# Kernel tuning notes

Hardware: AMD Instinct MI355X
Metric: run time of the kernel (lower is better)

Reference implementation:

```python
import jax, jax.numpy as jnp
import numpy as np

N_NODES = 100000
N_EDGES = 3200000
N_GRAPHS = 1024
D = 64
STEPS_PROP = 6
STEPS_S2S = 6


def setup_inputs() -> dict:
    key = jax.random.key(0)
    ks = jax.random.split(key, 16)
    inp = {}
    inp['x'] = jax.random.normal(ks[0], (N_NODES, 15), dtype=jnp.float32)
    inp['edge_index'] = jax.random.randint(ks[1], (2, N_EDGES), 0, N_NODES, dtype=jnp.int64 if jax.config.jax_enable_x64 else jnp.int32)
    inp['batch'] = jnp.sort(jax.random.randint(ks[2], (N_NODES,), 0, N_GRAPHS, dtype=jnp.int64 if jax.config.jax_enable_x64 else jnp.int32))
    s = 0.1
    inp['W0'] = jax.random.normal(ks[3], (15, D), dtype=jnp.float32) * s
    inp['b0'] = jax.random.normal(ks[4], (D,), dtype=jnp.float32) * s
    inp['Wc'] = jax.random.normal(ks[5], (D, D), dtype=jnp.float32) * s
    inp['bc'] = jax.random.normal(ks[6], (D,), dtype=jnp.float32) * s
    inp['Wih'] = jax.random.normal(ks[7], (4 * D, 2 * D), dtype=jnp.float32) * s
    inp['Whh'] = jax.random.normal(ks[8], (4 * D, D), dtype=jnp.float32) * s
    inp['bih'] = jax.random.normal(ks[9], (4 * D,), dtype=jnp.float32) * s
    inp['bhh'] = jax.random.normal(ks[10], (4 * D,), dtype=jnp.float32) * s
    inp['W1'] = jax.random.normal(ks[11], (2 * D, D), dtype=jnp.float32) * s
    inp['b1'] = jax.random.normal(ks[12], (D,), dtype=jnp.float32) * s
    inp['W2'] = jax.random.normal(ks[13], (D, 12), dtype=jnp.float32) * s
    inp['b2'] = jax.random.normal(ks[14], (12,), dtype=jnp.float32) * s
    return inp


def _gcn_forward(x, edge_index, batch, W0, b0, Wc, bc, Wih, Whh, bih, bhh, W1, b1, W2, b2):
    N = x.shape[0]
    # GCNConv normalization with self-loops (PyG semantics): A_hat = D^-1/2 (A+I) D^-1/2
    loops = jnp.arange(N, dtype=edge_index.dtype)
    row = jnp.concatenate([edge_index[0], loops])  # source
    col = jnp.concatenate([edge_index[1], loops])  # target
    deg = jax.ops.segment_sum(jnp.ones_like(col, dtype=x.dtype), col, num_segments=N)
    dinv = jnp.where(deg > 0, jax.lax.rsqrt(jnp.maximum(deg, 1e-30)), 0.0)
    norm = dinv[row] * dinv[col]  # [E+N]

    out = jax.nn.relu(x @ W0 + b0)  # [N, D]
    for _ in range(STEPS_PROP):
        h = out @ Wc  # transform first
        msg = h[row] * norm[:, None]  # gather along edges
        out = jax.nn.relu(jax.ops.segment_sum(msg, col, num_segments=N) + bc)

    # Set2Set pooling
    B = N_GRAPHS
    d = out.shape[1]
    h_l = jnp.zeros((B, d), dtype=out.dtype)
    c_l = jnp.zeros((B, d), dtype=out.dtype)
    q_star = jnp.zeros((B, 2 * d), dtype=out.dtype)
    for _ in range(STEPS_S2S):
        gates = q_star @ Wih.T + h_l @ Whh.T + bih + bhh  # [B, 4d]
        i_g, f_g, g_g, o_g = jnp.split(gates, 4, axis=1)
        c_l = jax.nn.sigmoid(f_g) * c_l + jax.nn.sigmoid(i_g) * jnp.tanh(g_g)
        h_l = jax.nn.sigmoid(o_g) * jnp.tanh(c_l)
        q = h_l  # [B, d]
        e = jnp.sum(out * q[batch], axis=-1)  # [N]
        m = jax.ops.segment_max(e, batch, num_segments=B)
        a_num = jnp.exp(e - m[batch])
        denom = jax.ops.segment_sum(a_num, batch, num_segments=B)
        a = a_num / denom[batch]
        r = jax.ops.segment_sum(a[:, None] * out, batch, num_segments=B)  # [B, d]
        q_star = jnp.concatenate([q, r], axis=-1)

    y = jax.nn.relu(q_star @ W1 + b1)
    return y @ W2 + b2  # [B, 12]


def reference(x, edge_index, batch, W0, b0, Wc, bc, Wih, Whh, bih, bhh, W1, b1, W2, b2):
    return _gcn_forward(x, edge_index, batch, W0, b0, Wc, bc, Wih, Whh, bih, bhh, W1, b1, W2, b2)
```

## Files before the change

kernel.cpp:

```cpp
#include <hip/hip_runtime.h>
#include <hip/hip_fp16.h>
#include <math.h>

#define ND 64
constexpr int BKT_SHIFT = 9;
constexpr int BKT_MASK = (1 << BKT_SHIFT) - 1;
constexpr int BCUR_PAD = 16;
constexpr int STG_TILE = 8192;
constexpr int S2S_CAP = 144;

__device__ __forceinline__ float sigmoidf_(float x){ return 1.f/(1.f+__expf(-x)); }
__device__ __forceinline__ __half2 h2lo(uint2 v){ return *reinterpret_cast<__half2*>(&v.x); }
__device__ __forceinline__ __half2 h2hi(uint2 v){ return *reinterpret_cast<__half2*>(&v.y); }
__device__ __forceinline__ __half2 shxor_h2(__half2 h, int off){
  unsigned u = *reinterpret_cast<unsigned*>(&h);
  u = __shfl_xor(u, off, 64);
  return *reinterpret_cast<__half2*>(&u);
}

__global__ void k_bhist(const int* __restrict__ col, int* __restrict__ bgcnt,
                        int E, int NBK){
  __shared__ int lhist[512];
  int t0 = blockIdx.x * STG_TILE;
  int t1 = t0 + STG_TILE; if (t1 > E) t1 = E;
  for (int i = threadIdx.x; i < NBK; i += 256) lhist[i] = 0;
  __syncthreads();
  for (int i = t0 + threadIdx.x; i < t1; i += 256)
    atomicAdd(&lhist[col[i] >> BKT_SHIFT], 1);
  __syncthreads();
  for (int i = threadIdx.x; i < NBK; i += 256)
    if (lhist[i] > 0) atomicAdd(&bgcnt[i], lhist[i]);
}

__global__ void k_bscan(const int* __restrict__ bgcnt, int* __restrict__ bstart,
                        int* __restrict__ rowptr, int NBK, int E, int N){
  __shared__ int tmp[256];
  int t = threadIdx.x;
  int v = (t < NBK) ? bgcnt[t] : 0;
  tmp[t] = v; __syncthreads();
  for (int off=1; off<256; off<<=1){
    int u = (t>=off) ? tmp[t-off] : 0;
    __syncthreads();
    tmp[t] += u;
    __syncthreads();
  }
  if (t <= NBK) bstart[t] = (t==0) ? 0 : tmp[t-1];
  if (t == 0) rowptr[N] = E;
}

__global__ void k_bcinit(const int* __restrict__ bstart, int* __restrict__ bcur, int NBK){
  int b = blockIdx.x*blockDim.x + threadIdx.x;
  if (b < NBK) bcur[b*BCUR_PAD] = bstart[b];
}

__global__ void k_stage2(const int* __restrict__ row, const int* __restrict__ col,
                         int* __restrict__ bcur, unsigned* __restrict__ pairs,
                         int E, int NBK){
  __shared__ int lhist[512];
  __shared__ int lbase[512];
  int t0 = blockIdx.x * STG_TILE;
  int t1 = t0 + STG_TILE; if (t1 > E) t1 = E;
  for (int i = threadIdx.x; i < NBK; i += 256) lhist[i] = 0;
  __syncthreads();
  for (int i = t0 + threadIdx.x; i < t1; i += 256)
    atomicAdd(&lhist[col[i] >> BKT_SHIFT], 1);
  __syncthreads();
  for (int i = threadIdx.x; i < NBK; i += 256){
    int c = lhist[i];
    lbase[i] = (c > 0) ? atomicAdd(&bcur[i*BCUR_PAD], c) : 0;
    lhist[i] = 0;
  }
  __syncthreads();
  for (int i = t0 + threadIdx.x; i < t1; i += 256){
    int d = col[i];
    int b = d >> BKT_SHIFT;
    int pos = lbase[b] + atomicAdd(&lhist[b], 1);
    pairs[pos] = ((unsigned)row[i] << BKT_SHIFT) | (unsigned)(d & BKT_MASK);
  }
}

__global__ void k_place(const unsigned* __restrict__ pairs, const int* __restrict__ bstart,
                        int* __restrict__ rowptr, float* __restrict__ dinv,
                        int* __restrict__ csr, int N){
  __shared__ int h[1 << BKT_SHIFT];
  __shared__ int excl[1 << BKT_SHIFT];
  __shared__ int tsum[256];
  int b = blockIdx.x;
  int base = b << BKT_SHIFT;
  int nend = base + (1 << BKT_SHIFT); if (nend > N) nend = N;
  int cnt = nend - base;
  int t = threadIdx.x;
  int s = bstart[b], e = bstart[b+1];

  h[2*t] = 0; h[2*t+1] = 0;
  __syncthreads();
  for (int i = s + t; i < e; i += 256)
    atomicAdd(&h[pairs[i] & BKT_MASK], 1);
  __syncthreads();
  int a0 = h[2*t], a1 = h[2*t+1];
  tsum[t] = a0 + a1;
  __syncthreads();
  for (int off=1; off<256; off<<=1){
    int u = (t>=off) ? tsum[t-off] : 0;
    __syncthreads();
    tsum[t] += u;
    __syncthreads();
  }
  int base0 = (t==0) ? 0 : tsum[t-1];
  excl[2*t]   = base0;
  excl[2*t+1] = base0 + a0;
  __syncthreads();
  for (int c = t; c < cnt; c += 256){
    int deg = h[c];
    rowptr[base + c] = s + excl[c];
    dinv[base + c] = rsqrtf((float)(deg + 1));
  }
  __syncthreads();
  for (int c = t; c < cnt; c += 256) h[c] = s + excl[c];
  __syncthreads();
  for (int i = s + t; i < e; i += 256){
    unsigned p = pairs[i];
    int pos = atomicAdd(&h[p & BKT_MASK], 1);
    csr[pos] = (int)(p >> BKT_SHIFT);
  }
}

__global__ void k_input(const float* __restrict__ x, const float* __restrict__ W0,
                        const float* __restrict__ b0, const float* __restrict__ dinv,
                        __half* __restrict__ s, int N){
  __shared__ float w0s[15*ND];
  __shared__ float b0s[ND];
  int tid = threadIdx.x;
  for (int i=tid; i<15*ND; i+=256) w0s[i] = W0[i];
  if (tid < ND) b0s[tid] = b0[tid];
  __syncthreads();
  int node = blockIdx.x*4 + (tid>>6);
  int f = tid & 63;
  if (node < N){
    float acc = b0s[f];
    const float* xr = x + (size_t)node*15;
    #pragma unroll
    for (int k=0;k<15;k++) acc += xr[k]*w0s[k*ND+f];
    s[(size_t)node*ND+f] = __float2half_rn(dinv[node]*fmaxf(acc, 0.f));
  }
}

__global__ void k_prop(const __half* __restrict__ sbuf, const int* __restrict__ rowptr,
                       const int* __restrict__ csr, const float* __restrict__ dinv,
                       const float* __restrict__ Wc, const float* __restrict__ bc,
                       __half* __restrict__ s_new, __half* __restrict__ outh,
                       int N, int wout){
  __shared__ float wcs[ND*ND];
  __shared__ float xs[16][ND];
  __shared__ float bcs[ND];
  const uint2* g8 = (const uint2*)sbuf;
  int tid = threadIdx.x;
  for (int i=tid; i<ND*ND; i+=256) wcs[i] = Wc[i];
  if (tid < ND) bcs[tid] = bc[tid];
  int nb = blockIdx.x*16;
  int wv = tid>>6, lane = tid&63;
  int grp = lane>>4, li = lane&15;

  for (int q=0; q<4; ++q){
    int node = nb + wv*4 + q;
    float val = 0.f;
    if (node < N){
      int s = rowptr[node], e = rowptr[node+1];
      __half2 z = __float2half2_rn(0.f);
      __half2 a0x=z,a0y=z, a1x=z,a1y=z, a2x=z,a2y=z, a3x=z,a3y=z;
      int i = s;
      for (; i + 16 <= e; i += 16){
        int s0 = csr[i +  0 + grp];
        int s1 = csr[i +  4 + grp];
        int s2 = csr[i +  8 + grp];
        int s3 = csr[i + 12 + grp];
        uint2 v0 = g8[(size_t)s0*16 + li];
        uint2 v1 = g8[(size_t)s1*16 + li];
        uint2 v2 = g8[(size_t)s2*16 + li];
        uint2 v3 = g8[(size_t)s3*16 + li];
        a0x = __hadd2(a0x, h2lo(v0)); a0y = __hadd2(a0y, h2hi(v0));
        a1x = __hadd2(a1x, h2lo(v1)); a1y = __hadd2(a1y, h2hi(v1));
        a2x = __hadd2(a2x, h2lo(v2)); a2y = __hadd2(a2y, h2hi(v2));
        a3x = __hadd2(a3x, h2lo(v3)); a3y = __hadd2(a3y, h2hi(v3));
      }
      for (; i + 4 <= e; i += 4){
        int s0 = csr[i + grp];
        uint2 v0 = g8[(size_t)s0*16 + li];
        a0x = __hadd2(a0x, h2lo(v0)); a0y = __hadd2(a0y, h2hi(v0));
      }
      int r = e - i;
      if (grp < r){
        int s0 = csr[i + grp];
        uint2 v0 = g8[(size_t)s0*16 + li];
        a1x = __hadd2(a1x, h2lo(v0)); a1y = __hadd2(a1y, h2hi(v0));
      }
      __half2 sxh = __hadd2(__hadd2(a0x,a1x), __hadd2(a2x,a3x));
      __half2 syh = __hadd2(__hadd2(a0y,a1y), __hadd2(a2y,a3y));
      sxh = __hadd2(sxh, shxor_h2(sxh, 16));
      syh = __hadd2(syh, shxor_h2(syh, 16));
      sxh = __hadd2(sxh, shxor_h2(sxh, 32));
      syh = __hadd2(syh, shxor_h2(syh, 32));
      uint2 sv = g8[(size_t)node*16 + li];
      sxh = __hadd2(sxh, h2lo(sv));
      syh = __hadd2(syh, h2hi(sv));
      val = (grp==0) ? __half2float(__low2half(sxh))
          : (grp==1) ? __half2float(__high2half(sxh))
          : (grp==2) ? __half2float(__low2half(syh))
          :            __half2float(__high2half(syh));
    }
    xs[wv*4+q][4*li+grp] = val;
  }
  __syncthreads();

  int f = tid&63, nq = tid>>6;
  float acc0=0.f, acc1=0.f, acc2=0.f, acc3=0.f;
  #pragma unroll 16
  for (int k=0;k<ND;k++){
    float w = wcs[k*ND+f];
    acc0 += w*xs[nq*4+0][k];
    acc1 += w*xs[nq*4+1][k];
    acc2 += w*xs[nq*4+2][k];
    acc3 += w*xs[nq*4+3][k];
  }
  int n0 = nb + nq*4;
  float bcf = bcs[f];
  #pragma unroll
  for (int j=0; j<4; ++j){
    int node = n0 + j;
    if (node < N){
      float a = (j==0)?acc0:(j==1)?acc1:(j==2)?acc2:acc3;
      float dn = dinv[node];
      float r = fmaxf(dn*a + bcf, 0.f);
      if (wout) outh[(size_t)node*ND+f] = __float2half_rn(r);
      else      s_new[(size_t)node*ND+f] = __float2half_rn(dn*r);
    }
  }
}

__global__ void k_goff(const int* __restrict__ batch, int* __restrict__ goff, int N, int B){
  int i = blockIdx.x*blockDim.x + threadIdx.x;
  if (i >= N) return;
  int b = batch[i];
  if (i == 0){ for (int g2=0; g2<=b; ++g2) goff[g2]=0; }
  else {
    int bp = batch[i-1];
    for (int g2=bp+1; g2<=b; ++g2) goff[g2]=i;
  }
  if (i == N-1){ for (int g2=b+1; g2<=B; ++g2) goff[g2]=N; }
}

__global__ void k_wprep(const float* __restrict__ Wih, const float* __restrict__ Whh,
                        const float* __restrict__ bih, const float* __restrict__ bhh,
                        unsigned* __restrict__ WC2, unsigned* __restrict__ WR2,
                        float* __restrict__ bsum){
  int k2 = blockIdx.x;
  int j  = threadIdx.x;
  int k = 2*k2;
  float c0 = Wih[(size_t)j*128 + k]     + Whh[(size_t)j*64 + k];
  float c1 = Wih[(size_t)j*128 + k + 1] + Whh[(size_t)j*64 + k + 1];
  float r0 = Wih[(size_t)j*128 + 64 + k];
  float r1 = Wih[(size_t)j*128 + 64 + k + 1];
  __half2 hc = __halves2half2(__float2half_rn(c0), __float2half_rn(c1));
  __half2 hr = __halves2half2(__float2half_rn(r0), __float2half_rn(r1));
  WC2[k2*256 + j] = *reinterpret_cast<unsigned*>(&hc);
  WR2[k2*256 + j] = *reinterpret_cast<unsigned*>(&hr);
  if (k2 == 0) bsum[j] = bih[j] + bhh[j];
}

__global__ void k_s2s(const __half* __restrict__ nodef, const int* __restrict__ goff,
                      const unsigned* __restrict__ WC2g, const unsigned* __restrict__ WR2g,
                      const float* __restrict__ bsum,
                      const float* __restrict__ W1, const float* __restrict__ b1,
                      const float* __restrict__ W2, const float* __restrict__ b2,
                      float* __restrict__ outy, int B){
  __shared__ unsigned lwc[32*256];
  __shared__ unsigned lwr[32*256];
  __shared__ float qsr[4][128];
  __shared__ float clr[4][64];
  __shared__ float gat[4][256];
  __shared__ float redm[4][4], redd[4][4];
  __shared__ float redr[4][4][64];
  __shared__ float yy[4][64];
  __shared__ uint2 snode[4][S2S_CAP*17];

  int tid = threadIdx.x;
  int g0 = blockIdx.x*4;
  int lane = tid&63, wv = tid>>6;
  int grp = lane>>4, li = lane&15;

  for (int i=tid; i<32*256; i+=256){ lwc[i] = WC2g[i]; lwr[i] = WR2g[i]; }
  for (int i=tid; i<4*128; i+=256) qsr[i>>7][i&127] = 0.f;
  if (tid < 256){ clr[tid>>6][tid&63] = 0.f; }

  int mygraph = g0 + wv;
  int s = 0, cnt = 0;
  const uint2* nf = (const uint2*)nodef;
  bool lds_ok = false;
  if (mygraph < B){
    s = goff[mygraph];
    cnt = goff[mygraph+1] - s;
    lds_ok = (cnt <= S2S_CAP);
    if (lds_ok){
      for (int i = lane; i < cnt*16; i += 64){
        int n = i >> 4, c = i & 15;
        snode[wv][n*17 + c] = nf[(size_t)(s+n)*16 + c];
      }
    }
  }
  float bsv = bsum[tid];
  __syncthreads();

  for (int step=0; step<6; ++step){
    {
      float a0=bsv, a1=bsv, a2=bsv, a3=bsv;
      for (int k2=0; k2<32; ++k2){
        unsigned uc = lwc[k2*256 + tid];
        unsigned ur = lwr[k2*256 + tid];
        float2 wc = __half22float2(*reinterpret_cast<__half2*>(&uc));
        float2 wr = __half22float2(*reinterpret_cast<__half2*>(&ur));
        float2 h0 = *(const float2*)&qsr[0][2*k2];
        float2 h1 = *(const float2*)&qsr[1][2*k2];
        float2 h2 = *(const float2*)&qsr[2][2*k2];
        float2 h3 = *(const float2*)&qsr[3][2*k2];
        float2 r0 = *(const float2*)&qsr[0][64+2*k2];
        float2 r1 = *(const float2*)&qsr[1][64+2*k2];
        float2 r2 = *(const float2*)&qsr[2][64+2*k2];
        float2 r3 = *(const float2*)&qsr[3][64+2*k2];
        a0 += wc.x*h0.x + wc.y*h0.y + wr.x*r0.x + wr.y*r0.y;
        a1 += wc.x*h1.x + wc.y*h1.y + wr.x*r1.x + wr.y*r1.y;
        a2 += wc.x*h2.x + wc.y*h2.y + wr.x*r2.x + wr.y*r2.y;
        a3 += wc.x*h3.x + wc.y*h3.y + wr.x*r3.x + wr.y*r3.y;
      }
      gat[0][tid]=a0; gat[1][tid]=a1; gat[2][tid]=a2; gat[3][tid]=a3;
    }
    __syncthreads();
    {
      int gg = tid>>6, d = tid&63;
      float ig = sigmoidf_(gat[gg][d]);
      float fg = sigmoidf_(gat[gg][64+d]);
      float gv = tanhf(gat[gg][128+d]);
      float og = sigmoidf_(gat[gg][192+d]);
      float c = fg*clr[gg][d] + ig*gv;
      float h = og*tanhf(c);
      clr[gg][d] = c;
      qsr[gg][d] = h;
    }
    __syncthreads();
    {
      float4 q4 = *(const float4*)&qsr[wv][4*li];
      float m = -3.0e38f, denom = 0.f;
      float r0=0.f, r1=0.f, r2=0.f, r3=0.f;
      if (lds_ok){
        for (int n = grp; n < cnt; n += 4){
          uint2 v = snode[wv][n*17 + li];
          float2 flo = __half22float2(h2lo(v));
          float2 fhi = __half22float2(h2hi(v));
          float p = flo.x*q4.x + flo.y*q4.y + fhi.x*q4.z + fhi.y*q4.w;
          p += __shfl_xor(p, 1, 64);
          p += __shfl_xor(p, 2, 64);
          p += __shfl_xor(p, 4, 64);
          p += __shfl_xor(p, 8, 64);
          if (p > m){
            float sc = __expf(m - p);
            denom *= sc; r0 *= sc; r1 *= sc; r2 *= sc; r3 *= sc;
            m = p;
          }
          float w = __expf(p - m);
          denom += w;
          r0 += w*flo.x; r1 += w*flo.y; r2 += w*fhi.x; r3 += w*fhi.y;
        }
      } else if (mygraph < B){
        for (int n = grp; n < cnt; n += 4){
          uint2 v = nf[(size_t)(s+n)*16 + li];
          float2 flo = __half22float2(h2lo(v));
          float2 fhi = __half22float2(h2hi(v));
          float p = flo.x*q4.x + flo.y*q4.y + fhi.x*q4.z + fhi.y*q4.w;
          p += __shfl_xor(p, 1, 64);
          p += __shfl_xor(p, 2, 64);
          p += __shfl_xor(p, 4, 64);
          p += __shfl_xor(p, 8, 64);
          if (p > m){
            float sc = __expf(m - p);
            denom *= sc; r0 *= sc; r1 *= sc; r2 *= sc; r3 *= sc;
            m = p;
          }
          float w = __expf(p - m);
          denom += w;
          r0 += w*flo.x; r1 += w*flo.y; r2 += w*fhi.x; r3 += w*fhi.y;
        }
      }
      if (li == 0){ redm[wv][grp] = m; redd[wv][grp] = denom; }
      redr[wv][grp][4*li+0] = r0;
      redr[wv][grp][4*li+1] = r1;
      redr[wv][grp][4*li+2] = r2;
      redr[wv][grp][4*li+3] = r3;
    }
    __syncthreads();
    {
      int gg = tid>>6, d = tid&63;
      float m0=redm[gg][0], m1=redm[gg][1], m2=redm[gg][2], m3=redm[gg][3];
      float mm = fmaxf(fmaxf(m0,m1), fmaxf(m2,m3));
      float s0=__expf(m0-mm), s1=__expf(m1-mm), s2=__expf(m2-mm), s3=__expf(m3-mm);
      float dt = redd[gg][0]*s0 + redd[gg][1]*s1 + redd[gg][2]*s2 + redd[gg][3]*s3;
      float rs = redr[gg][0][d]*s0 + redr[gg][1][d]*s1 + redr[gg][2][d]*s2 + redr[gg][3][d]*s3;
      qsr[gg][64+d] = (dt > 0.f) ? rs/dt : 0.f;
    }
    __syncthreads();
  }
  {
    int gg = tid>>6, f = tid&63;
    float acc = b1[f];
    for (int k=0;k<128;k++) acc += qsr[gg][k]*W1[k*64+f];
    yy[gg][f] = fmaxf(acc, 0.f);
  }
  __syncthreads();
  if (tid < 48){
    int gg = tid/12, o = tid%12;
    if (g0+gg < B){
      float a2 = b2[o];
      for (int k=0;k<64;k++) a2 += yy[gg][k]*W2[k*12+o];
      outy[(size_t)(g0+gg)*12+o] = a2;
    }
  }
}

extern "C" void kernel_launch(void* const* d_in, const int* in_sizes, int n_in,
                              void* d_out, int out_size, void* d_ws, size_t ws_size,
                              hipStream_t stream){
  const float* x    = (const float*)d_in[0];
  const int*   ei   = (const int*)d_in[1];
  const int*   batch= (const int*)d_in[2];
  const float* W0   = (const float*)d_in[3];
  const float* b0   = (const float*)d_in[4];
  const float* Wc   = (const float*)d_in[5];
  const float* bc   = (const float*)d_in[6];
  const float* Wih  = (const float*)d_in[7];
  const float* Whh  = (const float*)d_in[8];
  const float* bih  = (const float*)d_in[9];
  const float* bhh  = (const float*)d_in[10];
  const float* W1   = (const float*)d_in[11];
  const float* b1   = (const float*)d_in[12];
  const float* W2   = (const float*)d_in[13];
  const float* b2   = (const float*)d_in[14];
  float* yout = (float*)d_out;

  const int N = in_sizes[0]/15;
  const int E = in_sizes[1]/2;
  const int B = out_size/12;
  const int NBK = (N + (1<<BKT_SHIFT) - 1) >> BKT_SHIFT;
  const int* row = ei;
  const int* col = ei + E;

  char* ws = (char*)d_ws;
  size_t off = 0;
  auto alloc = [&](size_t bytes)->void*{
    void* p = ws + off; off = (off + bytes + 255) & ~(size_t)255; return p;
  };
  int*      bgcnt   = (int*)     alloc((size_t)(NBK+1)*4);
  int*      bstart  = (int*)     alloc((size_t)(NBK+1)*4);
  int*      bcur    = (int*)     alloc((size_t)NBK*BCUR_PAD*4);
  int*      rowptr  = (int*)     alloc((size_t)(N+1)*4);
  unsigned* pairs   = (unsigned*)alloc((size_t)E*4);
  int*      csr     = (int*)     alloc((size_t)E*4);
  float*    dinv    = (float*)   alloc((size_t)N*4);
  __half*   nodef   = (__half*)  alloc((size_t)N*ND*2);
  __half*   s_a     = (__half*)  alloc((size_t)N*ND*2);
  __half*   s_b     = (__half*)  alloc((size_t)N*ND*2);
  int*      goff    = (int*)     alloc((size_t)(B+1)*4);
  unsigned* WC2     = (unsigned*)alloc(32*256*4);
  unsigned* WR2     = (unsigned*)alloc(32*256*4);
  float*    bsum    = (float*)   alloc(256*4);
  (void)ws_size; (void)n_in;

  hipMemsetAsync(bgcnt, 0, (size_t)(NBK+1)*4, stream);

  int nstg = (E + STG_TILE - 1)/STG_TILE;
  k_bhist <<<nstg, 256, 0, stream>>>(col, bgcnt, E, NBK);
  k_bscan <<<1, 256, 0, stream>>>(bgcnt, bstart, rowptr, NBK, E, N);
  k_bcinit<<<(NBK+255)/256, 256, 0, stream>>>(bstart, bcur, NBK);
  k_stage2<<<nstg, 256, 0, stream>>>(row, col, bcur, pairs, E, NBK);
  k_place <<<NBK, 256, 0, stream>>>(pairs, bstart, rowptr, dinv, csr, N);

  k_input<<<(N+3)/4, 256, 0, stream>>>(x, W0, b0, dinv, s_a, N);
  __half* scur = s_a; __half* snxt = s_b;
  for (int s6=0; s6<6; ++s6){
    k_prop<<<(N+15)/16, 256, 0, stream>>>(scur, rowptr, csr, dinv,
                                          Wc, bc, snxt, nodef, N, (s6==5)?1:0);
    __half* t = scur; scur = snxt; snxt = t;
  }

  k_goff<<<(N+255)/256, 256, 0, stream>>>(batch, goff, N, B);
  k_wprep<<<32, 256, 0, stream>>>(Wih, Whh, bih, bhh, WC2, WR2, bsum);
  k_s2s<<<(B+3)/4, 256, 0, stream>>>(nodef, goff, WC2, WR2, bsum,
                                     W1, b1, W2, b2, yout, B);
}
```

Baseline: 839.1 us.

## Widen propagation gathers to 16-byte loads and store Wc as packed half2

The neighbor gather in k_prop now has each lane load a uint4 (8 halves), so one node row takes 8 lanes and a wave processes 8 edges per load, up from 4. The reduction across lanes now uses 4 half2 values over three xor shuffles. A new prep kernel packs Wc into half2 pairs, which halves the shared-memory staging footprint and the per-block load of Wc. The intent is fewer, wider memory transactions in the gather-bound loop and cheaper weight staging, at the cost of FP16 rounding on Wc and more shuffle work.

```diff
diff --git a/kernel.cpp b/kernel.cpp
--- a/kernel.cpp
+++ b/kernel.cpp
@@ -12,6 +12,7 @@
 __device__ __forceinline__ float sigmoidf_(float x){ return 1.f/(1.f+__expf(-x)); }
 __device__ __forceinline__ __half2 h2lo(uint2 v){ return *reinterpret_cast<__half2*>(&v.x); }
 __device__ __forceinline__ __half2 h2hi(uint2 v){ return *reinterpret_cast<__half2*>(&v.y); }
+__device__ __forceinline__ __half2 u2h2(unsigned u){ return *reinterpret_cast<__half2*>(&u); }
 __device__ __forceinline__ __half2 shxor_h2(__half2 h, int off){
   unsigned u = *reinterpret_cast<unsigned*>(&h);
   u = __shfl_xor(u, off, 64);
@@ -145,82 +146,99 @@
   }
 }
 
+__global__ void k_wcprep(const float* __restrict__ Wc, unsigned* __restrict__ wc2){
+  int i = blockIdx.x*256 + threadIdx.x;
+  if (i < 32*64){
+    int k2 = i >> 6, f = i & 63;
+    __half2 h = __halves2half2(__float2half_rn(Wc[(2*k2)*64 + f]),
+                               __float2half_rn(Wc[(2*k2+1)*64 + f]));
+    wc2[i] = *reinterpret_cast<unsigned*>(&h);
+  }
+}
+
 __global__ void k_prop(const __half* __restrict__ sbuf, const int* __restrict__ rowptr,
                        const int* __restrict__ csr, const float* __restrict__ dinv,
-                       const float* __restrict__ Wc, const float* __restrict__ bc,
+                       const unsigned* __restrict__ wc2, const float* __restrict__ bc,
                        __half* __restrict__ s_new, __half* __restrict__ outh,
                        int N, int wout){
-  __shared__ float wcs[ND*ND];
+  __shared__ unsigned wch[32*ND];
   __shared__ float xs[16][ND];
   __shared__ float bcs[ND];
-  const uint2* g8 = (const uint2*)sbuf;
+  const uint4* g16 = (const uint4*)sbuf;
   int tid = threadIdx.x;
-  for (int i=tid; i<ND*ND; i+=256) wcs[i] = Wc[i];
+  for (int i=tid; i<32*ND; i+=256) wch[i] = wc2[i];
   if (tid < ND) bcs[tid] = bc[tid];
   int nb = blockIdx.x*16;
   int wv = tid>>6, lane = tid&63;
-  int grp = lane>>4, li = lane&15;
+  int grp = lane>>3, li = lane&7;
 
   for (int q=0; q<4; ++q){
     int node = nb + wv*4 + q;
-    float val = 0.f;
+    __half2 z = __float2half2_rn(0.f);
+    __half2 A0=z,A1=z,A2=z,A3=z, B0=z,B1=z,B2=z,B3=z;
     if (node < N){
       int s = rowptr[node], e = rowptr[node+1];
-      __half2 z = __float2half2_rn(0.f);
-      __half2 a0x=z,a0y=z, a1x=z,a1y=z, a2x=z,a2y=z, a3x=z,a3y=z;
       int i = s;
       for (; i + 16 <= e; i += 16){
-        int s0 = csr[i +  0 + grp];
-        int s1 = csr[i +  4 + grp];
-        int s2 = csr[i +  8 + grp];
-        int s3 = csr[i + 12 + grp];
-        uint2 v0 = g8[(size_t)s0*16 + li];
-        uint2 v1 = g8[(size_t)s1*16 + li];
-        uint2 v2 = g8[(size_t)s2*16 + li];
-        uint2 v3 = g8[(size_t)s3*16 + li];
-        a0x = __hadd2(a0x, h2lo(v0)); a0y = __hadd2(a0y, h2hi(v0));
-        a1x = __hadd2(a1x, h2lo(v1)); a1y = __hadd2(a1y, h2hi(v1));
-        a2x = __hadd2(a2x, h2lo(v2)); a2y = __hadd2(a2y, h2hi(v2));
-        a3x = __hadd2(a3x, h2lo(v3)); a3y = __hadd2(a3y, h2hi(v3));
-      }
-      for (; i + 4 <= e; i += 4){
         int s0 = csr[i + grp];
-        uint2 v0 = g8[(size_t)s0*16 + li];
-        a0x = __hadd2(a0x, h2lo(v0)); a0y = __hadd2(a0y, h2hi(v0));
+        int s1 = csr[i + 8 + grp];
+        uint4 v0 = g16[(size_t)s0*8 + li];
+        uint4 v1 = g16[(size_t)s1*8 + li];
+        A0 = __hadd2(A0, u2h2(v0.x)); A1 = __hadd2(A1, u2h2(v0.y));
+        A2 = __hadd2(A2, u2h2(v0.z)); A3 = __hadd2(A3, u2h2(v0.w));
+        B0 = __hadd2(B0, u2h2(v1.x)); B1 = __hadd2(B1, u2h2(v1.y));
+        B2 = __hadd2(B2, u2h2(v1.z)); B3 = __hadd2(B3, u2h2(v1.w));
+      }
+      for (; i + 8 <= e; i += 8){
+        int s0 = csr[i + grp];
+        uint4 v0 = g16[(size_t)s0*8 + li];
+        A0 = __hadd2(A0, u2h2(v0.x)); A1 = __hadd2(A1, u2h2(v0.y));
+        A2 = __hadd2(A2, u2h2(v0.z)); A3 = __hadd2(A3, u2h2(v0.w));
       }
       int r = e - i;
       if (grp < r){
         int s0 = csr[i + grp];
-        uint2 v0 = g8[(size_t)s0*16 + li];
-        a1x = __hadd2(a1x, h2lo(v0)); a1y = __hadd2(a1y, h2hi(v0));
-      }
-      __half2 sxh = __hadd2(__hadd2(a0x,a1x), __hadd2(a2x,a3x));
-      __half2 syh = __hadd2(__hadd2(a0y,a1y), __hadd2(a2y,a3y));
-      sxh = __hadd2(sxh, shxor_h2(sxh, 16));
-      syh = __hadd2(syh, shxor_h2(syh, 16));
-      sxh = __hadd2(sxh, shxor_h2(sxh, 32));
-      syh = __hadd2(syh, shxor_h2(syh, 32));
-      uint2 sv = g8[(size_t)node*16 + li];
-      sxh = __hadd2(sxh, h2lo(sv));
-      syh = __hadd2(syh, h2hi(sv));
-      val = (grp==0) ? __half2float(__low2half(sxh))
-          : (grp==1) ? __half2float(__high2half(sxh))
-          : (grp==2) ? __half2float(__low2half(syh))
-          :            __half2float(__high2half(syh));
-    }
-    xs[wv*4+q][4*li+grp] = val;
+        uint4 v0 = g16[(size_t)s0*8 + li];
+        B0 = __hadd2(B0, u2h2(v0.x)); B1 = __hadd2(B1, u2h2(v0.y));
+        B2 = __hadd2(B2, u2h2(v0.z)); B3 = __hadd2(B3, u2h2(v0.w));
+      }
+      if (grp == 0){
+        uint4 sv = g16[(size_t)node*8 + li];
+        A0 = __hadd2(A0, u2h2(sv.x)); A1 = __hadd2(A1, u2h2(sv.y));
+        A2 = __hadd2(A2, u2h2(sv.z)); A3 = __hadd2(A3, u2h2(sv.w));
+      }
+    }
+    A0 = __hadd2(A0,B0); A1 = __hadd2(A1,B1); A2 = __hadd2(A2,B2); A3 = __hadd2(A3,B3);
+    #pragma unroll
+    for (int off=8; off<=32; off<<=1){
+      A0 = __hadd2(A0, shxor_h2(A0, off));
+      A1 = __hadd2(A1, shxor_h2(A1, off));
+      A2 = __hadd2(A2, shxor_h2(A2, off));
+      A3 = __hadd2(A3, shxor_h2(A3, off));
+    }
+    if (grp == 0){
+      float2 f0 = __half22float2(A0);
+      float2 f1 = __half22float2(A1);
+      float2 f2 = __half22float2(A2);
+      float2 f3 = __half22float2(A3);
+      float* xp = &xs[wv*4+q][8*li];
+      xp[0]=f0.x; xp[1]=f0.y; xp[2]=f1.x; xp[3]=f1.y;
+      xp[4]=f2.x; xp[5]=f2.y; xp[6]=f3.x; xp[7]=f3.y;
+    }
   }
   __syncthreads();
 
   int f = tid&63, nq = tid>>6;
   float acc0=0.f, acc1=0.f, acc2=0.f, acc3=0.f;
-  #pragma unroll 16
-  for (int k=0;k<ND;k++){
-    float w = wcs[k*ND+f];
-    acc0 += w*xs[nq*4+0][k];
-    acc1 += w*xs[nq*4+1][k];
-    acc2 += w*xs[nq*4+2][k];
-    acc3 += w*xs[nq*4+3][k];
+  #pragma unroll 8
+  for (int k2=0;k2<32;k2++){
+    unsigned u = wch[k2*ND+f];
+    float2 w = __half22float2(u2h2(u));
+    int k = 2*k2;
+    acc0 += w.x*xs[nq*4+0][k] + w.y*xs[nq*4+0][k+1];
+    acc1 += w.x*xs[nq*4+1][k] + w.y*xs[nq*4+1][k+1];
+    acc2 += w.x*xs[nq*4+2][k] + w.y*xs[nq*4+2][k+1];
+    acc3 += w.x*xs[nq*4+3][k] + w.y*xs[nq*4+3][k+1];
   }
   int n0 = nb + nq*4;
   float bcf = bcs[f];
@@ -470,6 +488,7 @@
   unsigned* WC2     = (unsigned*)alloc(32*256*4);
   unsigned* WR2     = (unsigned*)alloc(32*256*4);
   float*    bsum    = (float*)   alloc(256*4);
+  unsigned* wc2     = (unsigned*)alloc(32*64*4);
   (void)ws_size; (void)n_in;
 
   hipMemsetAsync(bgcnt, 0, (size_t)(NBK+1)*4, stream);
@@ -481,11 +500,12 @@
   k_stage2<<<nstg, 256, 0, stream>>>(row, col, bcur, pairs, E, NBK);
   k_place <<<NBK, 256, 0, stream>>>(pairs, bstart, rowptr, dinv, csr, N);
 
+  k_wcprep<<<8, 256, 0, stream>>>(Wc, wc2);
   k_input<<<(N+3)/4, 256, 0, stream>>>(x, W0, b0, dinv, s_a, N);
   __half* scur = s_a; __half* snxt = s_b;
   for (int s6=0; s6<6; ++s6){
     k_prop<<<(N+15)/16, 256, 0, stream>>>(scur, rowptr, csr, dinv,
-                                          Wc, bc, snxt, nodef, N, (s6==5)?1:0);
+                                          wc2, bc, snxt, nodef, N, (s6==5)?1:0);
     __half* t = scur; scur = snxt; snxt = t;
   }
 
```

New measurement: 991.4 us. 1.18x slower.
